# Optimization experiments

Hardware: AMD Instinct MI355X
Metric: run time of the kernel (lower is better)

## Reference

```python
import jax, jax.numpy as jnp
import numpy as np

B, S, D, H, DFF = 2, 2048, 768, 12, 3072
DK = D // H
LN_EPS = 1e-5

def _row_norm(x):
    # L2-normalize along last dim (torch F.normalize semantics)
    n = jnp.sqrt(jnp.sum(x * x, axis=-1, keepdims=True))
    return x / jnp.maximum(n, 1e-12)

def _layer_norm(x, gamma, beta):
    mu = jnp.mean(x, axis=-1, keepdims=True)
    var = jnp.mean((x - mu) ** 2, axis=-1, keepdims=True)
    return (x - mu) * jax.lax.rsqrt(var + LN_EPS) * gamma + beta

def setup_inputs() -> dict:
    key = jax.random.key(0)
    ks = jax.random.split(key, 16)
    sd = 1.0 / np.sqrt(D)
    sf = 1.0 / np.sqrt(DFF)
    inp = {
        "x": jax.random.normal(ks[0], (B, S, D), jnp.float32),
        "Wq": jax.random.uniform(ks[1], (D, D), jnp.float32, -sd, sd),
        "bq": jnp.zeros((D,), jnp.float32),
        "Wk": jax.random.uniform(ks[2], (D, D), jnp.float32, -sd, sd),
        "bk": jnp.zeros((D,), jnp.float32),
        "Wv": jax.random.uniform(ks[3], (D, D), jnp.float32, -sd, sd),
        "bv": jnp.zeros((D,), jnp.float32),
        "Wo": jax.random.uniform(ks[4], (D, D), jnp.float32, -sd, sd),
        "bo": jnp.zeros((D,), jnp.float32),
        "W1": jax.random.uniform(ks[5], (D, DFF), jnp.float32, -sd, sd),
        "b1": jnp.zeros((DFF,), jnp.float32),
        "W2": jax.random.uniform(ks[6], (DFF, D), jnp.float32, -sf, sf),
        "b2": jnp.zeros((D,), jnp.float32),
        "gamma": jnp.ones((D,), jnp.float32),
        "beta": jnp.zeros((D,), jnp.float32),
    }
    return inp

def reference(x, Wq, bq, Wk, bk, Wv, bv, Wo, bo, W1, b1, W2, b2, gamma, beta):
    b, s = x.shape[0], x.shape[1]
    # QKV projections, split into heads: [B,H,S,DK]
    def heads(y):
        return y.reshape(b, s, H, DK).transpose(0, 2, 1, 3)
    Q = heads(x @ Wq + bq)
    K = heads(x @ Wk + bk)
    V = heads(x @ Wv + bv)
    Qn = _row_norm(Q)
    Kn = _row_norm(K)
    scores = jnp.einsum("bhqd,bhkd->bhqk", Qn, Kn)
    attn = scores * scores  # squared dot-product, no softmax
    out = jnp.einsum("bhqk,bhkd->bhqd", attn, V)
    out = out.transpose(0, 2, 1, 3).reshape(b, s, D)
    attn_out = out @ Wo + bo
    x = _layer_norm(x + attn_out, gamma, beta)
    # FFN with exact GELU
    h = jax.nn.gelu(x @ W1 + b1, approximate=False)
    ff = h @ W2 + b2
    x = _layer_norm(x + ff, gamma, beta)  # norm1 reused
    return x
```

## Files before the change

### kernel.cpp

```cpp
#include <hip/hip_runtime.h>
#include <math.h>

using bf16   = __bf16;
using bf16x8 = __attribute__((ext_vector_type(8))) __bf16;
using bf16x4 = __attribute__((ext_vector_type(4))) __bf16;
using f32x4  = __attribute__((ext_vector_type(4))) float;

constexpr int S_   = 2048;
constexpr int D_   = 768;
constexpr int DFF_ = 3072;
constexpr int M_   = 4096;
constexpr int BH_  = 24;

__device__ __forceinline__ f32x4 mfma16(bf16x8 a, bf16x8 b, f32x4 c) {
    return __builtin_amdgcn_mfma_f32_16x16x32_bf16(a, b, c, 0, 0, 0);
}

__device__ __forceinline__ void gload16(const bf16* g, bf16* l) {
    __builtin_amdgcn_global_load_lds(
        (const __attribute__((address_space(1))) void*)g,
        (__attribute__((address_space(3))) void*)l, 16, 0, 0);
}

template<int N> __device__ __forceinline__ void wait_vmcnt() {
    if constexpr (N == 0)      asm volatile("s_waitcnt vmcnt(0)" ::: "memory");
    else if constexpr (N == 4) asm volatile("s_waitcnt vmcnt(4)" ::: "memory");
    else if constexpr (N == 6) asm volatile("s_waitcnt vmcnt(6)" ::: "memory");
    else if constexpr (N == 8) asm volatile("s_waitcnt vmcnt(8)" ::: "memory");
    else static_assert(N == 0, "unsupported vmcnt");
}
__device__ __forceinline__ void wait_lgkm0() {
    asm volatile("s_waitcnt lgkmcnt(0)" ::: "memory");
}

__device__ __forceinline__ int xcd_swz(int orig, int nwg) {
    return (orig & 7) * (nwg >> 3) + (orig >> 3);
}

__device__ __forceinline__ float gelu_f(float v) {
    float y = 1.5957691f * (v + 0.044715f * v * v * v);
    return v / (1.0f + __expf(-y));
}

__global__ __launch_bounds__(256)
void pack_x_kernel(const float* __restrict__ x, bf16* __restrict__ xb) {
    const int i = blockIdx.x * 256 + threadIdx.x;
    float4 v = ((const float4*)x)[i];
    bf16x4 o;
    o[0] = (bf16)v.x; o[1] = (bf16)v.y; o[2] = (bf16)v.z; o[3] = (bf16)v.w;
    ((bf16x4*)xb)[i] = o;
}

__global__ __launch_bounds__(256)
void merge_ao_kernel(const bf16* __restrict__ a, const bf16* __restrict__ b,
                     bf16* __restrict__ o) {
    const long i = ((long)blockIdx.x * 256 + threadIdx.x) * 8;
    bf16x8 va = *(const bf16x8*)&a[i];
    bf16x8 vb = *(const bf16x8*)&b[i];
    bf16x8 vo;
#pragma unroll
    for (int j = 0; j < 8; j++) vo[j] = (bf16)((float)va[j] + (float)vb[j]);
    *(bf16x8*)&o[i] = vo;
}

template<bool FIRST>
__global__ __launch_bounds__(256)
void merge_ln_kernel(const bf16* __restrict__ pp, const float* __restrict__ bias,
                     const float* __restrict__ residf, const bf16* __restrict__ residb,
                     const float* __restrict__ gamma, const float* __restrict__ beta,
                     float* __restrict__ outf, bf16* __restrict__ outb) {
    __shared__ float sa[4], sb[4];
    const int row = blockIdx.x, t = threadIdx.x;
    const bf16* p0 = pp + (long)row * 768;
    const bf16* p1 = pp + (long)M_ * 768 + (long)row * 768;
    float v[3];
#pragma unroll
    for (int i = 0; i < 3; i++) {
        const int c = t + i * 256;
        float y = (float)p0[c] + (float)p1[c] + bias[c];
        if (FIRST) y += residf[(long)row * 768 + c];
        else       y += (float)residb[(long)row * 768 + c];
        v[i] = y;
    }
    float s  = v[0] + v[1] + v[2];
    float ss = v[0] * v[0] + v[1] * v[1] + v[2] * v[2];
#pragma unroll
    for (int o = 32; o; o >>= 1) { s += __shfl_xor(s, o); ss += __shfl_xor(ss, o); }
    if ((t & 63) == 0) { sa[t >> 6] = s; sb[t >> 6] = ss; }
    __syncthreads();
    s  = sa[0] + sa[1] + sa[2] + sa[3];
    ss = sb[0] + sb[1] + sb[2] + sb[3];
    const float mu   = s * (1.0f / 768.0f);
    const float var  = ss * (1.0f / 768.0f) - mu * mu;
    const float rstd = rsqrtf(var + 1e-5f);
#pragma unroll
    for (int i = 0; i < 3; i++) {
        const int c = t + i * 256;
        const float ov = (v[i] - mu) * rstd * gamma[c] + beta[c];
        if (FIRST) outb[(long)row * 768 + c] = (bf16)ov;
        else       outf[(long)row * 768 + c] = ov;
    }
}

__global__ __launch_bounds__(256)
void wt_all_kernel(const float* __restrict__ Wq, const float* __restrict__ Wk,
                   const float* __restrict__ Wv, const float* __restrict__ Wo,
                   const float* __restrict__ W1, const float* __restrict__ W2,
                   bf16* __restrict__ Wqkvt, bf16* __restrict__ Wot,
                   bf16* __restrict__ W1t, bf16* __restrict__ W2t) {
    int bid = blockIdx.x;
    const float* in; bf16* out; int K, N, t;
    if (bid < 576) {
        int m = bid / 144; t = bid % 144; K = 768; N = 768;
        in  = (m == 0) ? Wq : (m == 1) ? Wk : (m == 2) ? Wv : Wo;
        out = (m == 3) ? Wot : Wqkvt + (size_t)m * 768 * 768;
    } else if (bid < 1152) {
        t = bid - 576; K = 768; N = 3072; in = W1; out = W1t;
    } else {
        t = bid - 1152; K = 3072; N = 768; in = W2; out = W2t;
    }
    const int ntx = N / 64;
    const int n0 = (t % ntx) * 64, k0 = (t / ntx) * 64;

    __shared__ __align__(16) bf16 T[64][72];
    const int tt = threadIdx.x;
    const int r  = tt >> 2, c0 = (tt & 3) * 16;
    const float* src = in + (size_t)(k0 + r) * N + n0 + c0;
#pragma unroll
    for (int j = 0; j < 16; j += 4) {
        float4 v = *(const float4*)(src + j);
        T[r][c0 + j + 0] = (bf16)v.x;
        T[r][c0 + j + 1] = (bf16)v.y;
        T[r][c0 + j + 2] = (bf16)v.z;
        T[r][c0 + j + 3] = (bf16)v.w;
    }
    __syncthreads();
    bf16x8 o0, o1;
#pragma unroll
    for (int j = 0; j < 8; j++) { o0[j] = T[c0 + j][r]; o1[j] = T[c0 + 8 + j][r]; }
    bf16* dst = out + (size_t)(n0 + r) * K + k0 + c0;
    *(bf16x8*)(dst)     = o0;
    *(bf16x8*)(dst + 8) = o1;
}

template<int EPI, int K, int BM, int BN, int WR, int WC, int KSPLIT>
__global__ __launch_bounds__(256)
void gemm_bt(const bf16* __restrict__ A, const bf16* __restrict__ Bt,
             const float* __restrict__ bias0, const float* __restrict__ bias1,
             const float* __restrict__ bias2,
             bf16* __restrict__ outb,
             bf16* __restrict__ qo, bf16* __restrict__ ko, bf16* __restrict__ vo) {
    constexpr int MR  = BM / WR / 16;
    constexpr int NR  = BN / WC / 16;
    constexpr int GA  = BM / 32;
    constexpr int GB  = BN / 32;
    constexpr int NPT = GA + GB;
    constexpr int KS  = K / KSPLIT;
    constexpr int NCOL = (EPI == 0) ? 2304 : (EPI == 2) ? 3072 : 768;
    constexpr int NBX  = NCOL / BN;
    __shared__ __align__(16) bf16 Al[2 * BM * 64];
    __shared__ __align__(16) bf16 Bl[2 * BN * 64];
    const int tid  = threadIdx.x;
    const int lane = tid & 63, w = tid >> 6;
    const int wr = w / WC, wc = w % WC;
    const int wg = xcd_swz(blockIdx.x, gridDim.x);
    const int ks = wg % KSPLIT;
    const int tt = wg / KSPLIT;
    const int m0 = (tt / NBX) * BM, n0 = (tt % NBX) * BN;
    const int kb = ks * KS;
    const int g = lane >> 4, q = lane & 15;
    const int srow = lane >> 3;
    const int schunk = (((lane & 7) ^ ((lane >> 3) & 7))) * 8;

    f32x4 acc[MR][NR] = {};

    const bf16* gaA = A  + (long)(m0 + w * (BM / 4) + srow) * K + kb + schunk;
    const bf16* gaB = Bt + (long)(n0 + w * (BN / 4) + srow) * K + kb + schunk;

    auto stage = [&](int buf, int kt) {
#pragma unroll
        for (int i = 0; i < GA; i++)
            gload16(gaA + kt + (long)i * 8 * K,
                    &Al[buf * BM * 64 + (w * (BM / 4) + i * 8) * 64]);
#pragma unroll
        for (int i = 0; i < GB; i++)
            gload16(gaB + kt + (long)i * 8 * K,
                    &Bl[buf * BN * 64 + (w * (BN / 4) + i * 8) * 64]);
    };
    auto compute = [&](int buf) {
#pragma unroll
        for (int c = 0; c < 2; c++) {
            const int rch = ((c * 4 + g) ^ (q & 7)) * 8;
            bf16x8 af[MR], bfr[NR];
#pragma unroll
            for (int i = 0; i < MR; i++)
                af[i] = *(const bf16x8*)
                    &Al[buf * BM * 64 + (wr * (BM / WR) + i * 16 + q) * 64 + rch];
#pragma unroll
            for (int i = 0; i < NR; i++)
                bfr[i] = *(const bf16x8*)
                    &Bl[buf * BN * 64 + (wc * (BN / WC) + i * 16 + q) * 64 + rch];
#pragma unroll
            for (int mi = 0; mi < MR; mi++)
#pragma unroll
                for (int ni = 0; ni < NR; ni++)
                    acc[mi][ni] = mfma16(af[mi], bfr[ni], acc[mi][ni]);
        }
    };

    stage(0, 0);
    stage(1, 64);
    int cur = 0;
    for (int kt = 0; kt < KS - 64; kt += 64) {
        wait_vmcnt<NPT>();
        __builtin_amdgcn_s_barrier();
        compute(cur);
        wait_lgkm0();
        __builtin_amdgcn_s_barrier();
        if (kt + 128 < KS) stage(cur, kt + 128);
        cur ^= 1;
    }
    wait_vmcnt<0>();
    __builtin_amdgcn_s_barrier();
    compute(cur);

#pragma unroll
    for (int mi = 0; mi < MR; mi++) {
        if (EPI == 0) {
            const int col0  = n0 + wc * 64;
            const int which = (col0 >= 1536) ? 2 : (col0 >= 768 ? 1 : 0);
            const int row0  = m0 + wr * (BM / WR) + mi * 16 + g * 4;
            float val[NR][4];
#pragma unroll
            for (int ni = 0; ni < NR; ni++) {
                const int dd = col0 + ni * 16 + q - which * 768;
                const float bias = (which == 0 ? bias0 : which == 1 ? bias1 : bias2)[dd];
#pragma unroll
                for (int r = 0; r < 4; r++) val[ni][r] = acc[mi][ni][r] + bias;
            }
            if (which <= 1) {
#pragma unroll
                for (int r = 0; r < 4; r++) {
                    float ss = val[0][r] * val[0][r];
#pragma unroll
                    for (int ni = 1; ni < NR; ni++) ss += val[ni][r] * val[ni][r];
                    ss += __shfl_xor(ss, 1);
                    ss += __shfl_xor(ss, 2);
                    ss += __shfl_xor(ss, 4);
                    ss += __shfl_xor(ss, 8);
                    const float rn = 1.0f / fmaxf(sqrtf(ss), 1e-12f);
#pragma unroll
                    for (int ni = 0; ni < NR; ni++) val[ni][r] *= rn;
                }
            }
            const int dd0 = col0 - which * 768;
            const int hh  = dd0 >> 6;
            const long bh = (long)(row0 >> 11) * 12 + hh;
#pragma unroll
            for (int ni = 0; ni < NR; ni++) {
                const int dk = ni * 16 + q;
                if (which == 2) {
                    bf16x4 pv;
#pragma unroll
                    for (int r = 0; r < 4; r++) pv[r] = (bf16)val[ni][r];
                    *(bf16x4*)&vo[(bh * 64 + dk) * 2048 + (row0 & 2047)] = pv;
                } else {
                    bf16* dst = (which == 0) ? qo : ko;
#pragma unroll
                    for (int r = 0; r < 4; r++)
                        dst[(bh * 2048 + ((row0 + r) & 2047)) * 64 + dk] = (bf16)val[ni][r];
                }
            }
        } else if (EPI == 2) {
#pragma unroll
            for (int ni = 0; ni < NR; ni++) {
                const int col  = n0 + wc * (BN / WC) + ni * 16 + q;
                const int row0 = m0 + wr * (BM / WR) + mi * 16 + g * 4;
                const float bias = bias0[col];
#pragma unroll
                for (int r = 0; r < 4; r++) {
                    const float v = acc[mi][ni][r] + bias;
                    outb[(long)(row0 + r) * 3072 + col] = (bf16)gelu_f(v);
                }
            }
        } else {
#pragma unroll
            for (int ni = 0; ni < NR; ni++) {
                const int col  = n0 + wc * (BN / WC) + ni * 16 + q;
                const int row0 = m0 + wr * (BM / WR) + mi * 16 + g * 4;
#pragma unroll
                for (int r = 0; r < 4; r++)
                    outb[(long)ks * M_ * 768 + (long)(row0 + r) * 768 + col] =
                        (bf16)acc[mi][ni][r];
            }
        }
    }
}

__global__ __launch_bounds__(256, 3)
void attn_kernel(const bf16* __restrict__ Qn, const bf16* __restrict__ Kn,
                 const bf16* __restrict__ Vt, bf16* __restrict__ AOp) {
    const int wg  = xcd_swz(blockIdx.x, gridDim.x);
    const int bh  = wg >> 5;
    const int rem = wg & 31;
    const int kvhalf = rem >> 4;
    const int qblk   = rem & 15;
    const int tid = threadIdx.x, lane = tid & 63, w = tid >> 6;
    const int g = lane >> 4, q15 = lane & 15;
    const int qbase = qblk * 128 + w * 32;
    const int kv0   = kvhalf * 1024;
    constexpr int NT = 16;

    __shared__ __align__(16) bf16 Kl[2][64][72];
    __shared__ __align__(16) bf16 Vl[2][64][72];
    __shared__ __align__(16) bf16 Pl[4][16][72];
    bf16 (*Pw)[72] = Pl[w];

    const bf16* Qp = Qn + (long)bh * S_ * 64;
    const bf16* Kp = Kn + (long)bh * S_ * 64 + (long)kv0 * 64;
    const bf16* Vp = Vt + (long)bh * 64 * S_ + kv0;
    bf16* AOo = AOp + (long)kvhalf * M_ * D_;

    const int srow = tid >> 3, scol = (tid & 7) * 8;

    bf16x8 qf00 = *(const bf16x8*)&Qp[(long)(qbase + q15) * 64 + g * 8];
    bf16x8 qf01 = *(const bf16x8*)&Qp[(long)(qbase + q15) * 64 + 32 + g * 8];
    bf16x8 qf10 = *(const bf16x8*)&Qp[(long)(qbase + 16 + q15) * 64 + g * 8];
    bf16x8 qf11 = *(const bf16x8*)&Qp[(long)(qbase + 16 + q15) * 64 + 32 + g * 8];

    f32x4 o0[4] = {}, o1[4] = {};

    bf16x8 aK0, aK1, aV0, aV1, bK0, bK1, bV0, bV1;
    auto gloadA = [&](int kt) {
        aK0 = *(const bf16x8*)&Kp[(long)(kt + srow) * 64 + scol];
        aK1 = *(const bf16x8*)&Kp[(long)(kt + 32 + srow) * 64 + scol];
        aV0 = *(const bf16x8*)&Vp[(long)srow * S_ + kt + scol];
        aV1 = *(const bf16x8*)&Vp[(long)(32 + srow) * S_ + kt + scol];
    };
    auto gloadB = [&](int kt) {
        bK0 = *(const bf16x8*)&Kp[(long)(kt + srow) * 64 + scol];
        bK1 = *(const bf16x8*)&Kp[(long)(kt + 32 + srow) * 64 + scol];
        bV0 = *(const bf16x8*)&Vp[(long)srow * S_ + kt + scol];
        bV1 = *(const bf16x8*)&Vp[(long)(32 + srow) * S_ + kt + scol];
    };
    auto stageA = [&](int buf) {
        *(bf16x8*)&Kl[buf][srow][scol]      = aK0;
        *(bf16x8*)&Kl[buf][32 + srow][scol] = aK1;
        *(bf16x8*)&Vl[buf][srow][scol]      = aV0;
        *(bf16x8*)&Vl[buf][32 + srow][scol] = aV1;
    };
    auto stageB = [&](int buf) {
        *(bf16x8*)&Kl[buf][srow][scol]      = bK0;
        *(bf16x8*)&Kl[buf][32 + srow][scol] = bK1;
        *(bf16x8*)&Vl[buf][srow][scol]      = bV0;
        *(bf16x8*)&Vl[buf][32 + srow][scol] = bV1;
    };

    auto compute = [&](int cur) {
        bf16x8 kf[4][2];
#pragma unroll
        for (int ni = 0; ni < 4; ni++)
#pragma unroll
            for (int c = 0; c < 2; c++)
                kf[ni][c] = *(const bf16x8*)&Kl[cur][ni * 16 + q15][c * 32 + g * 8];
        f32x4 s0[4], s1[4];
#pragma unroll
        for (int ni = 0; ni < 4; ni++) {
            s0[ni] = mfma16(kf[ni][0], qf00, f32x4{0.f, 0.f, 0.f, 0.f});
            s0[ni] = mfma16(kf[ni][1], qf01, s0[ni]);
            s1[ni] = mfma16(kf[ni][0], qf10, f32x4{0.f, 0.f, 0.f, 0.f});
            s1[ni] = mfma16(kf[ni][1], qf11, s1[ni]);
        }
#pragma unroll
        for (int ni = 0; ni < 4; ni++) {
            bf16x4 p0;
#pragma unroll
            for (int r = 0; r < 4; r++) { float v = s0[ni][r]; p0[r] = (bf16)(v * v); }
            *(bf16x4*)&Pw[q15][ni * 16 + g * 4] = p0;
        }
        bf16x8 pf00 = *(const bf16x8*)&Pw[q15][g * 8];
        bf16x8 pf01 = *(const bf16x8*)&Pw[q15][32 + g * 8];
#pragma unroll
        for (int ni = 0; ni < 4; ni++) {
            bf16x4 p1;
#pragma unroll
            for (int r = 0; r < 4; r++) { float v = s1[ni][r]; p1[r] = (bf16)(v * v); }
            *(bf16x4*)&Pw[q15][ni * 16 + g * 4] = p1;
        }
        bf16x8 pf10 = *(const bf16x8*)&Pw[q15][g * 8];
        bf16x8 pf11 = *(const bf16x8*)&Pw[q15][32 + g * 8];
        bf16x8 vf[4][2];
#pragma unroll
        for (int ni = 0; ni < 4; ni++)
#pragma unroll
            for (int c = 0; c < 2; c++)
                vf[ni][c] = *(const bf16x8*)&Vl[cur][ni * 16 + q15][c * 32 + g * 8];
#pragma unroll
        for (int ni = 0; ni < 4; ni++) {
            o0[ni] = mfma16(pf00, vf[ni][0], o0[ni]);
            o0[ni] = mfma16(pf01, vf[ni][1], o0[ni]);
            o1[ni] = mfma16(pf10, vf[ni][0], o1[ni]);
            o1[ni] = mfma16(pf11, vf[ni][1], o1[ni]);
        }
    };

    gloadA(0);
    stageA(0);
    gloadB(64);
    __syncthreads();
    for (int t = 0; t <= NT - 4; t += 2) {
        stageB(1);
        gloadA((t + 2) * 64);
        compute(0);
        __syncthreads();
        stageA(0);
        if (t + 3 < NT) gloadB((t + 3) * 64);
        compute(1);
        __syncthreads();
    }
    stageB(1);
    compute(0);
    __syncthreads();
    compute(1);

    const int b = bh / 12, h = bh % 12;
#pragma unroll
    for (int ni = 0; ni < 4; ni++)
#pragma unroll
        for (int r = 0; r < 4; r++) {
            const int s0r = qbase + g * 4 + r;
            AOo[((long)b * S_ + s0r) * D_ + h * 64 + ni * 16 + q15] = (bf16)o0[ni][r];
            const int s1r = qbase + 16 + g * 4 + r;
            AOo[((long)b * S_ + s1r) * D_ + h * 64 + ni * 16 + q15] = (bf16)o1[ni][r];
        }
}

extern "C" void kernel_launch(void* const* d_in, const int* in_sizes, int n_in,
                              void* d_out, int out_size, void* d_ws, size_t ws_size,
                              hipStream_t stream) {
    const float* x     = (const float*)d_in[0];
    const float* Wq    = (const float*)d_in[1];
    const float* bq    = (const float*)d_in[2];
    const float* Wk    = (const float*)d_in[3];
    const float* bk    = (const float*)d_in[4];
    const float* Wv    = (const float*)d_in[5];
    const float* bv    = (const float*)d_in[6];
    const float* Wo    = (const float*)d_in[7];
    const float* bo    = (const float*)d_in[8];
    const float* W1    = (const float*)d_in[9];
    const float* b1    = (const float*)d_in[10];
    const float* W2    = (const float*)d_in[11];
    const float* b2    = (const float*)d_in[12];
    const float* gamma = (const float*)d_in[13];
    const float* beta  = (const float*)d_in[14];

    char* p = (char*)d_ws;
    auto alloc = [&](size_t bytes) -> void* {
        void* r = p;
        p += (bytes + 255) & ~(size_t)255;
        return r;
    };
    bf16*  Xb    = (bf16*)alloc((size_t)M_ * D_ * 2);
    bf16*  Wqkvt = (bf16*)alloc((size_t)2304 * 768 * 2);
    bf16*  Wot   = (bf16*)alloc((size_t)768 * 768 * 2);
    bf16*  W1t   = (bf16*)alloc((size_t)3072 * 768 * 2);
    bf16*  W2t   = (bf16*)alloc((size_t)768 * 3072 * 2);
    bf16*  Qh    = (bf16*)alloc((size_t)BH_ * S_ * 64 * 2);
    bf16*  Kh    = (bf16*)alloc((size_t)BH_ * S_ * 64 * 2);
    bf16*  Vt    = (bf16*)alloc((size_t)BH_ * S_ * 64 * 2);
    bf16*  AOp   = (bf16*)alloc((size_t)2 * M_ * D_ * 2);
    bf16*  AO    = (bf16*)alloc((size_t)M_ * D_ * 2);
    bf16*  pp    = (bf16*)alloc((size_t)2 * M_ * 768 * 2);
    bf16*  x1b   = (bf16*)alloc((size_t)M_ * D_ * 2);
    bf16*  hbuf  = (bf16*)alloc((size_t)M_ * DFF_ * 2);

    pack_x_kernel<<<(M_ * D_) / 1024, 256, 0, stream>>>(x, Xb);
    wt_all_kernel<<<1728, 256, 0, stream>>>(Wq, Wk, Wv, Wo, W1, W2,
                                            Wqkvt, Wot, W1t, W2t);

    gemm_bt<0, 768, 64, 128, 2, 2, 1><<<64 * 18, 256, 0, stream>>>(
        Xb, Wqkvt, bq, bk, bv, nullptr, Qh, Kh, Vt);

    attn_kernel<<<2 * 16 * BH_, 256, 0, stream>>>(Qh, Kh, Vt, AOp);
    merge_ao_kernel<<<(M_ * D_) / 2048, 256, 0, stream>>>(
        AOp, AOp + (size_t)M_ * D_, AO);

    gemm_bt<1, 768, 64, 128, 2, 2, 2><<<64 * 6 * 2, 256, 0, stream>>>(
        AO, Wot, nullptr, nullptr, nullptr, pp, nullptr, nullptr, nullptr);
    merge_ln_kernel<true><<<M_, 256, 0, stream>>>(
        pp, bo, x, nullptr, gamma, beta, nullptr, x1b);

    gemm_bt<2, 768, 64, 128, 2, 2, 1><<<64 * 24, 256, 0, stream>>>(
        x1b, W1t, b1, nullptr, nullptr, hbuf, nullptr, nullptr, nullptr);

    gemm_bt<3, 3072, 64, 128, 2, 2, 2><<<64 * 6 * 2, 256, 0, stream>>>(
        hbuf, W2t, nullptr, nullptr, nullptr, pp, nullptr, nullptr, nullptr);
    merge_ln_kernel<false><<<M_, 256, 0, stream>>>(
        pp, b2, nullptr, x1b, gamma, beta, (float*)d_out, nullptr);
}
```

Measured before the change: 156.3 us.

## Software-pipeline attention loop across tiles and replace syncthreads with lgkm wait plus barrier

The attention inner loop is split into qk and pv stages so the second query block's P·V for one tile runs across the barrier into the next iteration, overlapping it with staging the next K/V tile. Full __syncthreads is replaced by an LDS-counter wait plus a raw s_barrier, which no longer waits on outstanding global loads. The goal is to hide barrier and LDS latency behind MFMA work. The risk is correctness of the per-wave P scratch reuse and the buffer ordering across the shifted stages.

```diff
diff --git a/kernel.cpp b/kernel.cpp
--- a/kernel.cpp
+++ b/kernel.cpp
@@ -329,8 +329,9 @@
     bf16x8 qf11 = *(const bf16x8*)&Qp[(long)(qbase + 16 + q15) * 64 + 32 + g * 8];
 
     f32x4 o0[4] = {}, o1[4] = {};
-
+    bf16x8 kf[4][2], vf[4][2];
     bf16x8 aK0, aK1, aV0, aV1, bK0, bK1, bV0, bV1;
+
     auto gloadA = [&](int kt) {
         aK0 = *(const bf16x8*)&Kp[(long)(kt + srow) * 64 + scol];
         aK1 = *(const bf16x8*)&Kp[(long)(kt + 32 + srow) * 64 + scol];
@@ -356,72 +357,77 @@
         *(bf16x8*)&Vl[buf][32 + srow][scol] = bV1;
     };
 
-    auto compute = [&](int cur) {
-        bf16x8 kf[4][2];
+    auto loadKf = [&](int cur) {
 #pragma unroll
         for (int ni = 0; ni < 4; ni++)
 #pragma unroll
             for (int c = 0; c < 2; c++)
                 kf[ni][c] = *(const bf16x8*)&Kl[cur][ni * 16 + q15][c * 32 + g * 8];
-        f32x4 s0[4], s1[4];
-#pragma unroll
-        for (int ni = 0; ni < 4; ni++) {
-            s0[ni] = mfma16(kf[ni][0], qf00, f32x4{0.f, 0.f, 0.f, 0.f});
-            s0[ni] = mfma16(kf[ni][1], qf01, s0[ni]);
-            s1[ni] = mfma16(kf[ni][0], qf10, f32x4{0.f, 0.f, 0.f, 0.f});
-            s1[ni] = mfma16(kf[ni][1], qf11, s1[ni]);
-        }
-#pragma unroll
-        for (int ni = 0; ni < 4; ni++) {
-            bf16x4 p0;
-#pragma unroll
-            for (int r = 0; r < 4; r++) { float v = s0[ni][r]; p0[r] = (bf16)(v * v); }
-            *(bf16x4*)&Pw[q15][ni * 16 + g * 4] = p0;
-        }
-        bf16x8 pf00 = *(const bf16x8*)&Pw[q15][g * 8];
-        bf16x8 pf01 = *(const bf16x8*)&Pw[q15][32 + g * 8];
-#pragma unroll
-        for (int ni = 0; ni < 4; ni++) {
-            bf16x4 p1;
-#pragma unroll
-            for (int r = 0; r < 4; r++) { float v = s1[ni][r]; p1[r] = (bf16)(v * v); }
-            *(bf16x4*)&Pw[q15][ni * 16 + g * 4] = p1;
-        }
-        bf16x8 pf10 = *(const bf16x8*)&Pw[q15][g * 8];
-        bf16x8 pf11 = *(const bf16x8*)&Pw[q15][32 + g * 8];
-        bf16x8 vf[4][2];
+    };
+    auto loadVf = [&](int cur) {
 #pragma unroll
         for (int ni = 0; ni < 4; ni++)
 #pragma unroll
             for (int c = 0; c < 2; c++)
                 vf[ni][c] = *(const bf16x8*)&Vl[cur][ni * 16 + q15][c * 32 + g * 8];
+    };
+    auto qk = [&](bf16x8 qa, bf16x8 qb) {
+        f32x4 s[4];
 #pragma unroll
         for (int ni = 0; ni < 4; ni++) {
-            o0[ni] = mfma16(pf00, vf[ni][0], o0[ni]);
-            o0[ni] = mfma16(pf01, vf[ni][1], o0[ni]);
-            o1[ni] = mfma16(pf10, vf[ni][0], o1[ni]);
-            o1[ni] = mfma16(pf11, vf[ni][1], o1[ni]);
+            s[ni] = mfma16(kf[ni][0], qa, f32x4{0.f, 0.f, 0.f, 0.f});
+            s[ni] = mfma16(kf[ni][1], qb, s[ni]);
+        }
+#pragma unroll
+        for (int ni = 0; ni < 4; ni++) {
+            bf16x4 p4;
+#pragma unroll
+            for (int r = 0; r < 4; r++) { float v = s[ni][r]; p4[r] = (bf16)(v * v); }
+            *(bf16x4*)&Pw[q15][ni * 16 + g * 4] = p4;
+        }
+    };
+    auto pv = [&](f32x4 (&o)[4]) {
+        bf16x8 pf0 = *(const bf16x8*)&Pw[q15][g * 8];
+        bf16x8 pf1 = *(const bf16x8*)&Pw[q15][32 + g * 8];
+#pragma unroll
+        for (int ni = 0; ni < 4; ni++) {
+            o[ni] = mfma16(pf0, vf[ni][0], o[ni]);
+            o[ni] = mfma16(pf1, vf[ni][1], o[ni]);
         }
     };
 
     gloadA(0);
     stageA(0);
     gloadB(64);
-    __syncthreads();
-    for (int t = 0; t <= NT - 4; t += 2) {
+    wait_lgkm0(); __builtin_amdgcn_s_barrier();
+    stageB(1);
+    gloadA(2 * 64);
+    loadKf(0); qk(qf00, qf01);
+    loadVf(0); pv(o0);
+    qk(qf10, qf11);
+
+    for (int t = 1; t <= NT - 3; t += 2) {
+        pv(o1);
+        wait_lgkm0(); __builtin_amdgcn_s_barrier();
+        stageA(0);
+        gloadB((t + 2) * 64);
+        loadKf(1); qk(qf00, qf01);
+        loadVf(1); pv(o0);
+        qk(qf10, qf11);
+        pv(o1);
+        wait_lgkm0(); __builtin_amdgcn_s_barrier();
         stageB(1);
-        gloadA((t + 2) * 64);
-        compute(0);
-        __syncthreads();
-        stageA(0);
-        if (t + 3 < NT) gloadB((t + 3) * 64);
-        compute(1);
-        __syncthreads();
-    }
-    stageB(1);
-    compute(0);
-    __syncthreads();
-    compute(1);
+        if (t + 3 < NT) gloadA((t + 3) * 64);
+        loadKf(0); qk(qf00, qf01);
+        loadVf(0); pv(o0);
+        qk(qf10, qf11);
+    }
+    pv(o1);
+    wait_lgkm0(); __builtin_amdgcn_s_barrier();
+    loadKf(1); qk(qf00, qf01);
+    loadVf(1); pv(o0);
+    qk(qf10, qf11);
+    pv(o1);
 
     const int b = bh / 12, h = bh % 12;
 #pragma unroll
```

Measured after the change: 156.2 us. No clear change (-0.0%).
